# Optimization experiments

Measured on AMD Instinct MI355X. Metric: run time of the kernel, lower is better.

Reference implementation:

```python
import jax, jax.numpy as jnp
import numpy as np

EPS = 1e-5  # BatchNorm1d default eps


def _proj_bn(x, W, gamma, beta, mean, var):
    # Conv1d(kernel=1, bias=False) == channel matmul, then inference BatchNorm1d.
    y = jnp.einsum('oc,bcn->bon', W, x)  # (B, C_out, N)
    scale = gamma / jnp.sqrt(var + EPS)  # (C_out,)
    shift = beta - mean * scale
    return y * scale[:, None] + shift[:, None]


def setup_inputs() -> dict:
    key = jax.random.key(0)
    ks = jax.random.split(key, 8)
    B, C, N = 8, 512, 2048
    inp = {
        'input': jax.random.normal(ks[0], (B, C, N), dtype=jnp.float32),
        'Wq': jax.random.normal(ks[1], (C, C), dtype=jnp.float32) * (1.0 / np.sqrt(C)),
        'gq': jnp.ones((C,), jnp.float32),
        'bq': jnp.zeros((C,), jnp.float32),
        'mq': jax.random.normal(ks[2], (C,), dtype=jnp.float32) * 0.1,
        'vq': jax.random.uniform(ks[3], (C,), dtype=jnp.float32) + 0.5,
        'Wk': jax.random.normal(ks[4], (C, C), dtype=jnp.float32) * (1.0 / np.sqrt(C)),
        'gk': jnp.ones((C,), jnp.float32),
        'bk': jnp.zeros((C,), jnp.float32),
        'mk': jax.random.normal(ks[5], (C,), dtype=jnp.float32) * 0.1,
        'vk': jax.random.uniform(ks[6], (C,), dtype=jnp.float32) + 0.5,
        'Wv': jax.random.normal(ks[7], (C, C), dtype=jnp.float32) * (1.0 / np.sqrt(C)),
        'gv': jnp.ones((C,), jnp.float32),
        'bv': jnp.zeros((C,), jnp.float32),
        'mv': jax.random.normal(jax.random.fold_in(key, 100), (C,), dtype=jnp.float32) * 0.1,
        'vv': jax.random.uniform(jax.random.fold_in(key, 101), (C,), dtype=jnp.float32) + 0.5,
    }
    return inp


def reference(input, Wq, gq, bq, mq, vq, Wk, gk, bk, mk, vk, Wv, gv, bv, mv, vv):
    q = _proj_bn(input, Wq, gq, bq, mq, vq)  # (B, C, N)
    k = _proj_bn(input, Wk, gk, bk, mk, vk)
    v = _proj_bn(input, Wv, gv, bv, mv, vv)
    # w[b, i, j] = sum_c q[b, c, i] * k[b, c, j]
    w = jnp.einsum('bci,bcj->bij', q, k)
    a = jax.nn.softmax(w, axis=-1)  # softmax over key axis j (dim 3 in torch)
    # c[b, c, i] = sum_j a[b, i, j] * v[b, c, j]  (== (v * w.softmax(3)).sum(3))
    return jnp.einsum('bij,bcj->bci', a, v)
```

## Files before the change

kernel.cpp:

```cpp
#include <hip/hip_runtime.h>
#include <cstdint>
#include <cstddef>

#define EPSV 1e-5f
constexpr int B_ = 8;
constexpr int C_ = 512;
constexpr int N_ = 2048;

typedef _Float16 f16x8 __attribute__((ext_vector_type(8)));
typedef float    f32x4 __attribute__((ext_vector_type(4)));

__device__ __forceinline__ unsigned short f16b(float f) {
    _Float16 h = (_Float16)f;
    return __builtin_bit_cast(unsigned short, h);
}

__device__ __forceinline__ void gload_lds16(const void* g, void* l) {
    __builtin_amdgcn_global_load_lds(
        (const __attribute__((address_space(1))) void*)g,
        (__attribute__((address_space(3))) void*)l, 16, 0, 0);
}

__global__ __launch_bounds__(256) void split_x_kernel(
    const float* __restrict__ x, unsigned short* __restrict__ xh)
{
    __shared__ float T[64][65];
    const int b = blockIdx.z, c0 = blockIdx.y * 64, n0 = blockIdx.x * 64;
    const float* xb = x + ((size_t)b * C_ + c0) * N_ + n0;
    const int tid = threadIdx.x;
    const int lr = tid >> 4;
    const int lcn = (tid & 15) * 4;
#pragma unroll
    for (int it = 0; it < 4; ++it) {
        float4 v = *(const float4*)&xb[(size_t)(lr + 16 * it) * N_ + lcn];
        T[lr + 16 * it][lcn + 0] = v.x;
        T[lr + 16 * it][lcn + 1] = v.y;
        T[lr + 16 * it][lcn + 2] = v.z;
        T[lr + 16 * it][lcn + 3] = v.w;
    }
    __syncthreads();
    const int n = tid >> 2, cb = (tid & 3) * 16;
    alignas(16) unsigned short h[16];
#pragma unroll
    for (int i = 0; i < 16; ++i)
        h[i] = f16b(T[cb + i][n]);
    const size_t o = ((size_t)b * N_ + n0 + n) * C_ + c0 + cb;
    *(uint4*)&xh[o]     = *(uint4*)&h[0];
    *(uint4*)&xh[o + 8] = *(uint4*)&h[8];
}

__global__ __launch_bounds__(256) void split_w_kernel(
    const float* __restrict__ W, unsigned short* __restrict__ wh)
{
    const int i = (blockIdx.x * 256 + threadIdx.x) * 4;
    float4 v = *(const float4*)&W[i];
    alignas(8) unsigned short h[4];
    h[0] = f16b(v.x); h[1] = f16b(v.y); h[2] = f16b(v.z); h[3] = f16b(v.w);
    *(ushort4*)&wh[i] = *(ushort4*)&h[0];
}

__global__ __launch_bounds__(512) void param_concat_kernel(
    const float* gq, const float* bq, const float* mq, const float* vq,
    const float* gk, const float* bk, const float* mk, const float* vk,
    float* sg, float* sb, float* sm, float* sv)
{
    const int i = threadIdx.x;
    sg[i] = gq[i];       sg[512 + i] = gk[i];
    sb[i] = bq[i];       sb[512 + i] = bk[i];
    sm[i] = mq[i];       sm[512 + i] = mk[i];
    sv[i] = vq[i];       sv[512 + i] = vk[i];
}

__global__ __launch_bounds__(256) void projv_mfma(
    const unsigned short* __restrict__ Ah, const unsigned short* __restrict__ Bh,
    int M, int N, int K, int lda, int ldb,
    long strideA, long strideB, long strideC,
    void* __restrict__ C0,
    const float* __restrict__ g, const float* __restrict__ bt,
    const float* __restrict__ mu, const float* __restrict__ var)
{
    __shared__ char smem[16384];

    const int id = blockIdx.x;
    const int bz = id & 7;
    const int s  = id >> 3;
    const int bx = s & 3, by = s >> 2;
    const int n0 = bx * 128;
    const int m0 = by * 128;

    const unsigned short* Ahb = Ah + (size_t)bz * strideA;
    const unsigned short* Bhb = Bh + (size_t)bz * strideB;

    const int tid = threadIdx.x;
    const int lane = tid & 63;
    const int wv = tid >> 6;
    const int wr = wv >> 1, wc = wv & 1;
    const int l4 = lane >> 4, l15 = lane & 15;
    const int srow = lane >> 2, scol8 = (lane & 3) * 8;

    f32x4 acc[4][4] = {};

    for (int k0 = 0; k0 < K; k0 += 32) {
#pragma unroll
        for (int cc = 0; cc < 2; ++cc) {
            const int c = wv * 2 + cc;
            const size_t aoff = (size_t)(m0 + c * 16 + srow) * lda + k0 + scol8;
            const size_t boff = (size_t)(n0 + c * 16 + srow) * ldb + k0 + scol8;
            gload_lds16(Ahb + aoff, smem + c * 1024);
            gload_lds16(Bhb + boff, smem + 8192 + c * 1024);
        }
        __syncthreads();

        f16x8 ah[4], bh[4];
#pragma unroll
        for (int f = 0; f < 4; ++f) {
            const int arow = wr * 64 + f * 16 + l15;
            const int brow = wc * 64 + f * 16 + l15;
            ah[f] = *(const f16x8*)(smem + arow * 64 + l4 * 16);
            bh[f] = *(const f16x8*)(smem + 8192 + brow * 64 + l4 * 16);
        }
#pragma unroll
        for (int fm = 0; fm < 4; ++fm)
#pragma unroll
            for (int fn = 0; fn < 4; ++fn)
                acc[fm][fn] = __builtin_amdgcn_mfma_f32_16x16x32_f16(
                    ah[fm], bh[fn], acc[fm][fn], 0, 0, 0);
        __syncthreads();
    }

#pragma unroll
    for (int fm = 0; fm < 4; ++fm) {
#pragma unroll
        for (int fn = 0; fn < 4; ++fn) {
            const int m = m0 + wr * 64 + fm * 16 + l4 * 4;
            const int n = n0 + wc * 64 + fn * 16 + l15;
            unsigned short* H = (unsigned short*)C0 + (size_t)bz * strideC;
            const float sc = g[n] * rsqrtf(var[n] + EPSV);
            const float sh = bt[n] - mu[n] * sc;
            alignas(8) unsigned short h4[4];
#pragma unroll
            for (int r = 0; r < 4; ++r)
                h4[r] = f16b(acc[fm][fn][r] * sc + sh);
            *(ushort4*)&H[(size_t)n * M + m] = *(ushort4*)&h4[0];
        }
    }
}

constexpr int EPI_QK = 0, EPI_PROJT = 2;

template <int EPI>
__global__ __launch_bounds__(512, 2) void qk256(
    const unsigned short* __restrict__ Ah, const unsigned short* __restrict__ Bh,
    int M, int N, int K, int lda, int ldb,
    long strideA, long strideB, long strideC,
    void* __restrict__ C0, float* __restrict__ ML,
    const float* __restrict__ g, const float* __restrict__ bt,
    const float* __restrict__ mu, const float* __restrict__ var)
{
    __shared__ char smem[131072];

    const int id = blockIdx.x;
    const int bz = id & 7;
    const int s  = id >> 3;
    const int bx = s & 7, by = s >> 3;
    const int n0 = bx * 256;
    const int m0 = by * 256;

    const unsigned short* Ahb = Ah + (size_t)bz * strideA;
    const unsigned short* Bhb = Bh + (size_t)bz * strideB;

    const int tid  = threadIdx.x;
    const int lane = tid & 63;
    const int wv   = tid >> 6;
    const int wr   = wv >> 2, wc = wv & 3;
    const int WRB  = wr * 128, WCB = wc * 64;
    const int l4 = lane >> 4, l15 = lane & 15;

    const int srow  = tid >> 3;
    const int sslot = ((tid & 7) ^ (srow & 7)) * 8;

#define STAGE(t)                                                              \
    {                                                                         \
        char* dst = smem + ((t) & 1) * 65536;                                 \
        const unsigned short* asrc =                                          \
            Ahb + (size_t)(m0 + srow) * lda + (t) * 64 + sslot;               \
        _Pragma("unroll")                                                     \
        for (int u = 0; u < 4; ++u)                                           \
            gload_lds16(asrc + (size_t)(u * 64) * lda,                        \
                        dst + u * 8192 + tid * 16);                           \
        const unsigned short* bsrc =                                          \
            Bhb + (size_t)(n0 + srow) * ldb + (t) * 64 + sslot;               \
        _Pragma("unroll")                                                     \
        for (int u = 0; u < 4; ++u)                                           \
            gload_lds16(bsrc + (size_t)(u * 64) * ldb,                        \
                        dst + 32768 + u * 8192 + tid * 16);                   \
    }

    f32x4 acc[8][4] = {};
    const int NT = K / 64;

    STAGE(0);

    for (int t = 0; t < NT; ++t) {
        char* cur = smem + (t & 1) * 65536;
        __builtin_amdgcn_s_barrier();
        if (t + 1 < NT) {
            STAGE(t + 1);
            asm volatile("s_waitcnt vmcnt(8)" ::: "memory");
        } else {
            asm volatile("s_waitcnt vmcnt(0)" ::: "memory");
        }
        __builtin_amdgcn_s_barrier();

        f16x8 ah[8][2], bh[4][2];
#pragma unroll
        for (int m = 0; m < 8; ++m) {
            const int row = WRB + m * 16 + l15;
#pragma unroll
            for (int kk = 0; kk < 2; ++kk)
                ah[m][kk] = *(const f16x8*)(cur + row * 128 +
                                            (((kk << 2) | l4) ^ (row & 7)) * 16);
        }
#pragma unroll
        for (int n = 0; n < 4; ++n) {
            const int row = WCB + n * 16 + l15;
#pragma unroll
            for (int kk = 0; kk < 2; ++kk)
                bh[n][kk] = *(const f16x8*)(cur + 32768 + row * 128 +
                                            (((kk << 2) | l4) ^ (row & 7)) * 16);
        }
        __builtin_amdgcn_s_setprio(1);
#pragma unroll
        for (int kk = 0; kk < 2; ++kk)
#pragma unroll
            for (int m = 0; m < 8; ++m)
#pragma unroll
                for (int n = 0; n < 4; ++n)
                    acc[m][n] = __builtin_amdgcn_mfma_f32_16x16x32_f16(
                        ah[m][kk], bh[n][kk], acc[m][n], 0, 0, 0);
        __builtin_amdgcn_s_setprio(0);
    }
#undef STAGE

    if constexpr (EPI == EPI_QK) {
        unsigned short* H = (unsigned short*)C0 + (size_t)bz * strideC;
        const int tcol = bx * 4 + wc;
        const size_t mbase = (((size_t)bz * 32 + tcol) * 2) * 2048;
#pragma unroll
        for (int m = 0; m < 8; ++m) {
#pragma unroll
            for (int r = 0; r < 4; ++r) {
                float mx = fmaxf(fmaxf(acc[m][0][r], acc[m][1][r]),
                                 fmaxf(acc[m][2][r], acc[m][3][r]));
#pragma unroll
                for (int off = 1; off < 16; off <<= 1)
                    mx = fmaxf(mx, __shfl_xor(mx, off));
                float pe[4];
                float s2 = 0.f;
#pragma unroll
                for (int n = 0; n < 4; ++n) {
                    pe[n] = __expf(acc[m][n][r] - mx);
                    s2 += pe[n];
                }
#pragma unroll
                for (int off = 1; off < 16; off <<= 1)
                    s2 += __shfl_xor(s2, off);
                const int rloc = WRB + m * 16 + l4 * 4 + r;
                if (l15 == 0) {
                    ML[mbase + m0 + rloc] = mx;
                    ML[mbase + 2048 + m0 + rloc] = s2;
                }
#pragma unroll
                for (int n = 0; n < 4; ++n)
                    H[(size_t)(m0 + rloc) * 2048 + n0 + WCB + n * 16 + l15] =
                        f16b(pe[n]);
            }
        }
    } else {
        unsigned short* H = (unsigned short*)C0 + (size_t)bz * strideC;
#pragma unroll
        for (int m = 0; m < 8; ++m) {
            const int mg = m0 + WRB + m * 16 + l4 * 4;
            float sc[4], sh[4];
#pragma unroll
            for (int r = 0; r < 4; ++r) {
                const int o = mg + r;
                sc[r] = g[o] * rsqrtf(var[o] + EPSV);
                sh[r] = bt[o] - mu[o] * sc[r];
            }
#pragma unroll
            for (int n = 0; n < 4; ++n) {
                const int ng = n0 + WCB + n * 16 + l15;
                alignas(8) unsigned short h4[4];
#pragma unroll
                for (int r = 0; r < 4; ++r)
                    h4[r] = f16b(acc[m][n][r] * sc[r] + sh[r]);
                *(ushort4*)&H[(size_t)ng * M + mg] = *(ushort4*)&h4[0];
            }
        }
    }
}

__global__ __launch_bounds__(512, 2) void pv256(
    const unsigned short* __restrict__ Ah, const unsigned short* __restrict__ Bh,
    int K, int lda, int ldb, long strideA, long strideB, long strideC,
    void* __restrict__ C0,
    const float* __restrict__ corr, const float* __restrict__ linv)
{
    constexpr int BUFSZ = 49152;
    __shared__ char smem[163840];

    const int id = blockIdx.x;
    const int bz = id & 7;
    const int s  = id >> 3;
    const int bx = s & 3, by = s >> 2;
    const int n0 = bx * 128;
    const int m0 = by * 256;

    const unsigned short* Ahb = Ah + (size_t)bz * strideA;
    const unsigned short* Bhb = Bh + (size_t)bz * strideB;

    const int tid  = threadIdx.x;
    const int lane = tid & 63;
    const int wv   = tid >> 6;
    const int wr   = wv >> 2, wc = wv & 3;
    const int WRB  = wr * 128, WCB = wc * 32;
    const int l4 = lane >> 4, l15 = lane & 15;

    const int srow = tid >> 3;
    const int sslot = ((tid & 7) ^ (srow & 7)) * 8;

    unsigned short* corrLds = (unsigned short*)(smem + 147456);
    for (int idx = tid; idx < 2048; idx += 512) {
        const int t = idx >> 6, i4 = (idx & 63) * 4;
        float4 c4 = *(const float4*)&corr[((size_t)bz * 32 + t) * 2048 + m0 + i4];
        alignas(8) unsigned short h4[4] =
            {f16b(c4.x), f16b(c4.y), f16b(c4.z), f16b(c4.w)};
        *(ushort4*)&corrLds[(size_t)t * 256 + i4] = *(ushort4*)&h4[0];
    }
    __syncthreads();

#define STAGE(t)                                                              \
    {                                                                         \
        char* dst = smem + ((t) % 3) * BUFSZ;                                 \
        const unsigned short* asrc =                                          \
            Ahb + (size_t)(m0 + srow) * lda + (t) * 64 + sslot;               \
        _Pragma("unroll")                                                     \
        for (int u = 0; u < 4; ++u)                                           \
            gload_lds16(asrc + (size_t)(u * 64) * lda,                        \
                        dst + u * 8192 + tid * 16);                           \
        const unsigned short* bsrc =                                          \
            Bhb + (size_t)(n0 + srow) * ldb + (t) * 64 + sslot;               \
        _Pragma("unroll")                                                     \
        for (int u = 0; u < 2; ++u)                                           \
            gload_lds16(bsrc + (size_t)(u * 64) * ldb,                        \
                        dst + 32768 + u * 8192 + tid * 16);                   \
    }

    f32x4 acc[8][2] = {};
    const int NT = K / 64;

    STAGE(0);
    STAGE(1);

    for (int t = 0; t < NT; ++t) {
        char* cur = smem + (t % 3) * BUFSZ;
        if (t + 2 < NT) {
            asm volatile("s_waitcnt vmcnt(6)" ::: "memory");
        } else {
            asm volatile("s_waitcnt vmcnt(0)" ::: "memory");
        }
        __builtin_amdgcn_s_barrier();
        asm volatile("" ::: "memory");
        if (t + 2 < NT) STAGE(t + 2);

        f16x8 ah[8][2], bh[2][2];
#pragma unroll
        for (int m = 0; m < 8; ++m) {
            const int row = WRB + m * 16 + l15;
#pragma unroll
            for (int kk = 0; kk < 2; ++kk)
                ah[m][kk] = *(const f16x8*)(cur + row * 128 +
                                            (((kk << 2) | l4) ^ (row & 7)) * 16);
        }
#pragma unroll
        for (int n = 0; n < 2; ++n) {
            const int row = WCB + n * 16 + l15;
#pragma unroll
            for (int kk = 0; kk < 2; ++kk)
                bh[n][kk] = *(const f16x8*)(cur + 32768 + row * 128 +
                                            (((kk << 2) | l4) ^ (row & 7)) * 16);
        }
#pragma unroll
        for (int m = 0; m < 8; ++m) {
            const _Float16 cf = ((const _Float16*)corrLds)
                [(size_t)t * 256 + WRB + m * 16 + l15];
            ah[m][0] = ah[m][0] * cf;
            ah[m][1] = ah[m][1] * cf;
        }
        __builtin_amdgcn_s_setprio(1);
#pragma unroll
        for (int kk = 0; kk < 2; ++kk)
#pragma unroll
            for (int m = 0; m < 8; ++m)
#pragma unroll
                for (int n = 0; n < 2; ++n)
                    acc[m][n] = __builtin_amdgcn_mfma_f32_16x16x32_f16(
                        ah[m][kk], bh[n][kk], acc[m][n], 0, 0, 0);
        __builtin_amdgcn_s_setprio(0);
    }
#undef STAGE

    float* Cb = (float*)C0 + (size_t)bz * strideC;
    const float* lb = linv + (size_t)bz * 2048;
#pragma unroll
    for (int m = 0; m < 8; ++m) {
        const int mrow = m0 + WRB + m * 16 + l4 * 4;
        float lv[4];
#pragma unroll
        for (int r = 0; r < 4; ++r)
            lv[r] = lb[mrow + r];
#pragma unroll
        for (int n = 0; n < 2; ++n) {
            const int col = n0 + WCB + n * 16 + l15;
            float4 o4 = make_float4(acc[m][n][0] * lv[0],
                                    acc[m][n][1] * lv[1],
                                    acc[m][n][2] * lv[2],
                                    acc[m][n][3] * lv[3]);
            *(float4*)&Cb[(size_t)col * 2048 + mrow] = o4;
        }
    }
}

__global__ __launch_bounds__(256) void ml_combine_kernel(
    const float* __restrict__ ml, float* __restrict__ corr,
    float* __restrict__ linv)
{
    const int idx = blockIdx.x * 256 + threadIdx.x;
    const int b = idx >> 11, i = idx & 2047;
    const float* base = ml + ((size_t)b * 32) * 2 * 2048 + i;
    float M = -3.0e38f;
#pragma unroll 8
    for (int t = 0; t < 32; ++t)
        M = fmaxf(M, base[(size_t)t * 4096]);
    float L = 0.f;
    float* cb = corr + (size_t)b * 32 * 2048 + i;
#pragma unroll 8
    for (int t = 0; t < 32; ++t) {
        const float c = __expf(base[(size_t)t * 4096] - M);
        L += c * base[(size_t)t * 4096 + 2048];
        cb[(size_t)t * 2048] = c;
    }
    linv[idx] = 1.0f / L;
}

extern "C" void kernel_launch(void* const* d_in, const int* in_sizes, int n_in,
                              void* d_out, int out_size, void* d_ws, size_t ws_size,
                              hipStream_t stream)
{
    (void)in_sizes; (void)n_in; (void)out_size; (void)ws_size;
    const float* x  = (const float*)d_in[0];
    const float* Wq = (const float*)d_in[1];
    const float* gq = (const float*)d_in[2];
    const float* bq = (const float*)d_in[3];
    const float* mq = (const float*)d_in[4];
    const float* vq = (const float*)d_in[5];
    const float* Wk = (const float*)d_in[6];
    const float* gk = (const float*)d_in[7];
    const float* bk = (const float*)d_in[8];
    const float* mk = (const float*)d_in[9];
    const float* vk = (const float*)d_in[10];
    const float* Wv = (const float*)d_in[11];
    const float* gv = (const float*)d_in[12];
    const float* bv = (const float*)d_in[13];
    const float* mv = (const float*)d_in[14];
    const float* vv = (const float*)d_in[15];
    float* out = (float*)d_out;

    const size_t MiB = 1048576;
    char* ws = (char*)d_ws;
    unsigned short* Wqh = (unsigned short*)(ws + 0 * 524288);
    unsigned short* Wkh = (unsigned short*)(ws + 1 * 524288);
    unsigned short* Wvh = (unsigned short*)(ws + 2 * 524288);
    unsigned short* vbf  = (unsigned short*)(ws + 2 * MiB);
    unsigned short* qkTh = (unsigned short*)(ws + 18 * MiB);
    unsigned short* xTh  = (unsigned short*)(ws + 50 * MiB);
    unsigned short* pbuf = (unsigned short*)(ws + 66 * MiB);
    float* mlbuf = (float*)(ws + 130 * MiB);
    float* corr  = (float*)(ws + 134 * MiB);
    float* linv  = (float*)(ws + 136 * MiB);
    float* sg = (float*)(ws + 136 * MiB + 65536);
    float* sb = sg + 1024;
    float* sm = sb + 1024;
    float* sv = sm + 1024;

    const long BS = (long)N_ * C_;
    const long QKS = (long)N_ * 1024;

    split_x_kernel<<<dim3(N_ / 64, C_ / 64, B_), 256, 0, stream>>>(x, xTh);
    split_w_kernel<<<dim3(256), 256, 0, stream>>>(Wq, Wqh);
    split_w_kernel<<<dim3(256), 256, 0, stream>>>(Wk, Wkh);
    split_w_kernel<<<dim3(256), 256, 0, stream>>>(Wv, Wvh);
    param_concat_kernel<<<dim3(1), 512, 0, stream>>>(
        gq, bq, mq, vq, gk, bk, mk, vk, sg, sb, sm, sv);

    qk256<EPI_PROJT><<<dim3(256), 512, 0, stream>>>(
        Wqh, xTh, 1024, 2048, 512, 512, 512, 0, BS, QKS, qkTh,
        nullptr, sg, sb, sm, sv);

    projv_mfma<<<dim3(512), 256, 0, stream>>>(
        xTh, Wvh, 2048, 512, 512, 512, 512, BS, 0, BS, vbf,
        gv, bv, mv, vv);

    qk256<EPI_QK><<<dim3(512), 512, 0, stream>>>(
        qkTh, qkTh + 512, 2048, 2048, 512, 1024, 1024, QKS, QKS,
        (long)N_ * N_, pbuf, mlbuf, nullptr, nullptr, nullptr, nullptr);

    ml_combine_kernel<<<dim3(B_ * N_ / 256), 256, 0, stream>>>(
        mlbuf, corr, linv);

    pv256<<<dim3(256), 512, 0, stream>>>(
        pbuf, vbf, 2048, 2048, 2048, (long)N_ * N_, BS, BS, out, corr, linv);
}
```

Measured before the change: 179.7 us.

## Split GEMM main loops into finer-grained quarter-tile stages with interleaved barriers

Restructures the qk256 and pv256 main loops so each K-tile is split into half-K sub-buffers with a 32-column swizzled LDS layout. Global-to-LDS loads are issued in quarter (qk) or half (pv) chunks between MFMA clusters, and each cluster is fenced by barriers with priority raising. This is a ping-pong style schedule that overlaps LDS reads, async global loads and MFMA more finely. pv256 moves from a triple to a double buffer, which lowers its LDS footprint. The intricate vmcnt accounting risks races or stalls if any count is wrong.

```diff
diff --git a/kernel.cpp b/kernel.cpp
--- a/kernel.cpp
+++ b/kernel.cpp
@@ -146,6 +146,15 @@
     }
 }
 
+#define BAR_PRE()                                                             \
+    __builtin_amdgcn_s_barrier();                                             \
+    asm volatile("s_waitcnt lgkmcnt(0)" ::: "memory");                        \
+    __builtin_amdgcn_sched_barrier(0);                                        \
+    __builtin_amdgcn_s_setprio(1)
+#define BAR_POST()                                                            \
+    __builtin_amdgcn_s_setprio(0);                                            \
+    __builtin_amdgcn_s_barrier()
+
 constexpr int EPI_QK = 0, EPI_PROJT = 2;
 
 template <int EPI>
@@ -176,71 +185,79 @@
     const int WRB  = wr * 128, WCB = wc * 64;
     const int l4 = lane >> 4, l15 = lane & 15;
 
-    const int srow  = tid >> 3;
-    const int sslot = ((tid & 7) ^ (srow & 7)) * 8;
-
-#define STAGE(t)                                                              \
-    {                                                                         \
-        char* dst = smem + ((t) & 1) * 65536;                                 \
-        const unsigned short* asrc =                                          \
-            Ahb + (size_t)(m0 + srow) * lda + (t) * 64 + sslot;               \
+    const int NT = K / 64;
+
+#define ISSUE_Q(sv_)                                                          \
+    if ((sv_) < 4 * NT) {                                                     \
+        const int T__ = (sv_) >> 2, j__ = (sv_) & 3;                          \
+        char* rb = smem + (T__ & 1) * 65536 + ((j__ & 1) ? 32768 : 0) +       \
+                   ((j__ >> 1) * 16384);                                      \
+        const unsigned short* src = (j__ & 1) ? Bhb : Ahb;                    \
+        const int base0 = (j__ & 1) ? n0 : m0;                                \
+        const int ld = (j__ & 1) ? ldb : lda;                                 \
+        const int colb = T__ * 64 + (j__ >> 1) * 32;                          \
         _Pragma("unroll")                                                     \
-        for (int u = 0; u < 4; ++u)                                           \
-            gload_lds16(asrc + (size_t)(u * 64) * lda,                        \
-                        dst + u * 8192 + tid * 16);                           \
-        const unsigned short* bsrc =                                          \
-            Bhb + (size_t)(n0 + srow) * ldb + (t) * 64 + sslot;               \
+        for (int u = 0; u < 2; ++u) {                                         \
+            const int L = u * 512 + tid;                                      \
+            const int row = L >> 2;                                           \
+            gload_lds16(src + (size_t)(base0 + row) * ld + colb +             \
+                            (((tid & 3) ^ (row & 3)) * 8),                    \
+                        rb + L * 16);                                         \
+        }                                                                     \
+    }
+
+#define RDA(kk, dst)                                                          \
+    _Pragma("unroll")                                                         \
+    for (int m_ = 0; m_ < 8; ++m_) {                                          \
+        const int r_ = WRB + m_ * 16 + l15;                                   \
+        dst[m_] = *(const f16x8*)(cur + (kk) * 16384 + r_ * 64 +              \
+                                  ((l4 ^ (r_ & 3)) * 16));                    \
+    }
+#define RDB(kk, nlo, dst)                                                     \
+    _Pragma("unroll")                                                         \
+    for (int n_ = 0; n_ < 2; ++n_) {                                          \
+        const int r_ = WCB + ((nlo) + n_) * 16 + l15;                         \
+        dst[n_] = *(const f16x8*)(cur + 32768 + (kk) * 16384 + r_ * 64 +      \
+                                  ((l4 ^ (r_ & 3)) * 16));                    \
+    }
+#define MFM(nlo)                                                              \
+    _Pragma("unroll")                                                         \
+    for (int m_ = 0; m_ < 8; ++m_)                                            \
         _Pragma("unroll")                                                     \
-        for (int u = 0; u < 4; ++u)                                           \
-            gload_lds16(bsrc + (size_t)(u * 64) * ldb,                        \
-                        dst + 32768 + u * 8192 + tid * 16);                   \
-    }
+        for (int n_ = 0; n_ < 2; ++n_)                                        \
+            acc[m_][(nlo) + n_] = __builtin_amdgcn_mfma_f32_16x16x32_f16(     \
+                ah[m_], bq[n_], acc[m_][(nlo) + n_], 0, 0, 0);
 
     f32x4 acc[8][4] = {};
-    const int NT = K / 64;
-
-    STAGE(0);
+    f16x8 ah[8], bq[2];
+
+    ISSUE_Q(0); ISSUE_Q(1); ISSUE_Q(2); ISSUE_Q(3); ISSUE_Q(4);
+    asm volatile("s_waitcnt vmcnt(6)" ::: "memory");
+    __builtin_amdgcn_s_barrier();
 
     for (int t = 0; t < NT; ++t) {
         char* cur = smem + (t & 1) * 65536;
-        __builtin_amdgcn_s_barrier();
-        if (t + 1 < NT) {
-            STAGE(t + 1);
-            asm volatile("s_waitcnt vmcnt(8)" ::: "memory");
-        } else {
-            asm volatile("s_waitcnt vmcnt(0)" ::: "memory");
-        }
-        __builtin_amdgcn_s_barrier();
-
-        f16x8 ah[8][2], bh[4][2];
-#pragma unroll
-        for (int m = 0; m < 8; ++m) {
-            const int row = WRB + m * 16 + l15;
-#pragma unroll
-            for (int kk = 0; kk < 2; ++kk)
-                ah[m][kk] = *(const f16x8*)(cur + row * 128 +
-                                            (((kk << 2) | l4) ^ (row & 7)) * 16);
-        }
-#pragma unroll
-        for (int n = 0; n < 4; ++n) {
-            const int row = WCB + n * 16 + l15;
-#pragma unroll
-            for (int kk = 0; kk < 2; ++kk)
-                bh[n][kk] = *(const f16x8*)(cur + 32768 + row * 128 +
-                                            (((kk << 2) | l4) ^ (row & 7)) * 16);
-        }
-        __builtin_amdgcn_s_setprio(1);
-#pragma unroll
-        for (int kk = 0; kk < 2; ++kk)
-#pragma unroll
-            for (int m = 0; m < 8; ++m)
-#pragma unroll
-                for (int n = 0; n < 4; ++n)
-                    acc[m][n] = __builtin_amdgcn_mfma_f32_16x16x32_f16(
-                        ah[m][kk], bh[n][kk], acc[m][n], 0, 0, 0);
-        __builtin_amdgcn_s_setprio(0);
-    }
-#undef STAGE
+        RDA(0, ah); RDB(0, 0, bq);
+        ISSUE_Q(4 * t + 5);
+        BAR_PRE(); MFM(0); BAR_POST();
+        RDB(0, 2, bq);
+        ISSUE_Q(4 * t + 6);
+        if (t + 1 < NT) { asm volatile("s_waitcnt vmcnt(6)" ::: "memory"); }
+        else            { asm volatile("s_waitcnt vmcnt(0)" ::: "memory"); }
+        BAR_PRE(); MFM(2); BAR_POST();
+        RDA(1, ah); RDB(1, 0, bq);
+        ISSUE_Q(4 * t + 7);
+        BAR_PRE(); MFM(0); BAR_POST();
+        RDB(1, 2, bq);
+        ISSUE_Q(4 * t + 8);
+        if (t + 2 < NT)       { asm volatile("s_waitcnt vmcnt(6)" ::: "memory"); }
+        else if (t + 2 == NT) { asm volatile("s_waitcnt vmcnt(4)" ::: "memory"); }
+        BAR_PRE(); MFM(2); BAR_POST();
+    }
+#undef ISSUE_Q
+#undef RDA
+#undef RDB
+#undef MFM
 
     if constexpr (EPI == EPI_QK) {
         unsigned short* H = (unsigned short*)C0 + (size_t)bz * strideC;
@@ -307,8 +324,7 @@
     void* __restrict__ C0,
     const float* __restrict__ corr, const float* __restrict__ linv)
 {
-    constexpr int BUFSZ = 49152;
-    __shared__ char smem[163840];
+    __shared__ char smem[114688];
 
     const int id = blockIdx.x;
     const int bz = id & 7;
@@ -327,10 +343,9 @@
     const int WRB  = wr * 128, WCB = wc * 32;
     const int l4 = lane >> 4, l15 = lane & 15;
 
-    const int srow = tid >> 3;
-    const int sslot = ((tid & 7) ^ (srow & 7)) * 8;
-
-    unsigned short* corrLds = (unsigned short*)(smem + 147456);
+    const int NT = K / 64;
+
+    unsigned short* corrLds = (unsigned short*)(smem + 98304);
     for (int idx = tid; idx < 2048; idx += 512) {
         const int t = idx >> 6, i4 = (idx & 63) * 4;
         float4 c4 = *(const float4*)&corr[((size_t)bz * 32 + t) * 2048 + m0 + i4];
@@ -340,76 +355,81 @@
     }
     __syncthreads();
 
-#define STAGE(t)                                                              \
-    {                                                                         \
-        char* dst = smem + ((t) % 3) * BUFSZ;                                 \
-        const unsigned short* asrc =                                          \
-            Ahb + (size_t)(m0 + srow) * lda + (t) * 64 + sslot;               \
+#define ISSUE_P(sv_)                                                          \
+    if ((sv_) < 2 * NT) {                                                     \
+        const int T__ = (sv_) >> 1, h__ = (sv_) & 1;                          \
+        char* rb = smem + (T__ & 1) * 49152;                                  \
+        const int colb = T__ * 64 + h__ * 32;                                 \
         _Pragma("unroll")                                                     \
-        for (int u = 0; u < 4; ++u)                                           \
-            gload_lds16(asrc + (size_t)(u * 64) * lda,                        \
-                        dst + u * 8192 + tid * 16);                           \
-        const unsigned short* bsrc =                                          \
-            Bhb + (size_t)(n0 + srow) * ldb + (t) * 64 + sslot;               \
+        for (int u = 0; u < 2; ++u) {                                         \
+            const int L = u * 512 + tid;                                      \
+            const int row = L >> 2;                                           \
+            gload_lds16(Ahb + (size_t)(m0 + row) * lda + colb +               \
+                            (((tid & 3) ^ (row & 3)) * 8),                    \
+                        rb + h__ * 16384 + L * 16);                           \
+        }                                                                     \
+        {                                                                     \
+            const int row = tid >> 2;                                         \
+            gload_lds16(Bhb + (size_t)(n0 + row) * ldb + colb +               \
+                            (((tid & 3) ^ (row & 3)) * 8),                    \
+                        rb + 32768 + h__ * 8192 + tid * 16);                  \
+        }                                                                     \
+    }
+
+#define RDAP(kk)                                                              \
+    _Pragma("unroll")                                                         \
+    for (int m_ = 0; m_ < 8; ++m_) {                                          \
+        const int r_ = WRB + m_ * 16 + l15;                                   \
+        ah[m_] = *(const f16x8*)(cur + (kk) * 16384 + r_ * 64 +               \
+                                 ((l4 ^ (r_ & 3)) * 16));                     \
+    }
+#define RDBP(kk)                                                              \
+    _Pragma("unroll")                                                         \
+    for (int n_ = 0; n_ < 2; ++n_) {                                          \
+        const int r_ = WCB + n_ * 16 + l15;                                   \
+        bq[n_] = *(const f16x8*)(cur + 32768 + (kk) * 8192 + r_ * 64 +        \
+                                 ((l4 ^ (r_ & 3)) * 16));                     \
+    }
+#define CORRM(t)                                                              \
+    _Pragma("unroll")                                                         \
+    for (int m_ = 0; m_ < 8; ++m_) {                                          \
+        const _Float16 cf = ((const _Float16*)corrLds)                        \
+            [(size_t)(t) * 256 + WRB + m_ * 16 + l15];                        \
+        ah[m_] = ah[m_] * cf;                                                 \
+    }
+#define MFMP()                                                                \
+    _Pragma("unroll")                                                         \
+    for (int m_ = 0; m_ < 8; ++m_)                                            \
         _Pragma("unroll")                                                     \
-        for (int u = 0; u < 2; ++u)                                           \
-            gload_lds16(bsrc + (size_t)(u * 64) * ldb,                        \
-                        dst + 32768 + u * 8192 + tid * 16);                   \
-    }
+        for (int n_ = 0; n_ < 2; ++n_)                                        \
+            acc[m_][n_] = __builtin_amdgcn_mfma_f32_16x16x32_f16(             \
+                ah[m_], bq[n_], acc[m_][n_], 0, 0, 0);
 
     f32x4 acc[8][2] = {};
-    const int NT = K / 64;
-
-    STAGE(0);
-    STAGE(1);
+    f16x8 ah[8], bq[2];
+
+    ISSUE_P(0); ISSUE_P(1); ISSUE_P(2);
+    asm volatile("s_waitcnt vmcnt(6)" ::: "memory");
+    __builtin_amdgcn_s_barrier();
 
     for (int t = 0; t < NT; ++t) {
-        char* cur = smem + (t % 3) * BUFSZ;
-        if (t + 2 < NT) {
-            asm volatile("s_waitcnt vmcnt(6)" ::: "memory");
-        } else {
-            asm volatile("s_waitcnt vmcnt(0)" ::: "memory");
-        }
-        __builtin_amdgcn_s_barrier();
-        asm volatile("" ::: "memory");
-        if (t + 2 < NT) STAGE(t + 2);
-
-        f16x8 ah[8][2], bh[2][2];
-#pragma unroll
-        for (int m = 0; m < 8; ++m) {
-            const int row = WRB + m * 16 + l15;
-#pragma unroll
-            for (int kk = 0; kk < 2; ++kk)
-                ah[m][kk] = *(const f16x8*)(cur + row * 128 +
-                                            (((kk << 2) | l4) ^ (row & 7)) * 16);
-        }
-#pragma unroll
-        for (int n = 0; n < 2; ++n) {
-            const int row = WCB + n * 16 + l15;
-#pragma unroll
-            for (int kk = 0; kk < 2; ++kk)
-                bh[n][kk] = *(const f16x8*)(cur + 32768 + row * 128 +
-                                            (((kk << 2) | l4) ^ (row & 7)) * 16);
-        }
-#pragma unroll
-        for (int m = 0; m < 8; ++m) {
-            const _Float16 cf = ((const _Float16*)corrLds)
-                [(size_t)t * 256 + WRB + m * 16 + l15];
-            ah[m][0] = ah[m][0] * cf;
-            ah[m][1] = ah[m][1] * cf;
-        }
-        __builtin_amdgcn_s_setprio(1);
-#pragma unroll
-        for (int kk = 0; kk < 2; ++kk)
-#pragma unroll
-            for (int m = 0; m < 8; ++m)
-#pragma unroll
-                for (int n = 0; n < 2; ++n)
-                    acc[m][n] = __builtin_amdgcn_mfma_f32_16x16x32_f16(
-                        ah[m][kk], bh[n][kk], acc[m][n], 0, 0, 0);
-        __builtin_amdgcn_s_setprio(0);
-    }
-#undef STAGE
+        char* cur = smem + (t & 1) * 49152;
+        RDAP(0); RDBP(0); CORRM(t);
+        ISSUE_P(2 * t + 3);
+        if (t + 1 < NT) { asm volatile("s_waitcnt vmcnt(6)" ::: "memory"); }
+        else            { asm volatile("s_waitcnt vmcnt(0)" ::: "memory"); }
+        BAR_PRE(); MFMP(); BAR_POST();
+        RDAP(1); RDBP(1); CORRM(t);
+        ISSUE_P(2 * t + 4);
+        if (t + 2 < NT)       { asm volatile("s_waitcnt vmcnt(6)" ::: "memory"); }
+        else if (t + 2 == NT) { asm volatile("s_waitcnt vmcnt(3)" ::: "memory"); }
+        BAR_PRE(); MFMP(); BAR_POST();
+    }
+#undef ISSUE_P
+#undef RDAP
+#undef RDBP
+#undef CORRM
+#undef MFMP
 
     float* Cb = (float*)C0 + (size_t)bz * strideC;
     const float* lb = linv + (size_t)bz * 2048;
```

New measurement: 201.3 us. 1.12x slower.

## Fuse V projection into the stacked Q/K projection GEMM launch

Applied to the files above, without the earlier changes.

Removes the separate small-tile projv_mfma kernel and stacks Wq, Wk and Wv into one contiguous weight matrix. The existing 256x256 qk256 projection kernel now runs over 1536 output rows (384 blocks), with a branch in the epilogue that writes V rows to the vbf buffer. This removes one launch and reuses the larger, more efficient tile for V. In exchange, the V epilogue stores each f16 element as a scalar, with lanes of a row writing consecutive addresses, where the Q/K path uses ushort4 vector stores, so V output writes may be less efficient.

```diff
diff --git a/kernel.cpp b/kernel.cpp
--- a/kernel.cpp
+++ b/kernel.cpp
@@ -62,88 +62,14 @@
 __global__ __launch_bounds__(512) void param_concat_kernel(
     const float* gq, const float* bq, const float* mq, const float* vq,
     const float* gk, const float* bk, const float* mk, const float* vk,
+    const float* gv, const float* bv, const float* mv, const float* vv,
     float* sg, float* sb, float* sm, float* sv)
 {
     const int i = threadIdx.x;
-    sg[i] = gq[i];       sg[512 + i] = gk[i];
-    sb[i] = bq[i];       sb[512 + i] = bk[i];
-    sm[i] = mq[i];       sm[512 + i] = mk[i];
-    sv[i] = vq[i];       sv[512 + i] = vk[i];
-}
-
-__global__ __launch_bounds__(256) void projv_mfma(
-    const unsigned short* __restrict__ Ah, const unsigned short* __restrict__ Bh,
-    int M, int N, int K, int lda, int ldb,
-    long strideA, long strideB, long strideC,
-    void* __restrict__ C0,
-    const float* __restrict__ g, const float* __restrict__ bt,
-    const float* __restrict__ mu, const float* __restrict__ var)
-{
-    __shared__ char smem[16384];
-
-    const int id = blockIdx.x;
-    const int bz = id & 7;
-    const int s  = id >> 3;
-    const int bx = s & 3, by = s >> 2;
-    const int n0 = bx * 128;
-    const int m0 = by * 128;
-
-    const unsigned short* Ahb = Ah + (size_t)bz * strideA;
-    const unsigned short* Bhb = Bh + (size_t)bz * strideB;
-
-    const int tid = threadIdx.x;
-    const int lane = tid & 63;
-    const int wv = tid >> 6;
-    const int wr = wv >> 1, wc = wv & 1;
-    const int l4 = lane >> 4, l15 = lane & 15;
-    const int srow = lane >> 2, scol8 = (lane & 3) * 8;
-
-    f32x4 acc[4][4] = {};
-
-    for (int k0 = 0; k0 < K; k0 += 32) {
-#pragma unroll
-        for (int cc = 0; cc < 2; ++cc) {
-            const int c = wv * 2 + cc;
-            const size_t aoff = (size_t)(m0 + c * 16 + srow) * lda + k0 + scol8;
-            const size_t boff = (size_t)(n0 + c * 16 + srow) * ldb + k0 + scol8;
-            gload_lds16(Ahb + aoff, smem + c * 1024);
-            gload_lds16(Bhb + boff, smem + 8192 + c * 1024);
-        }
-        __syncthreads();
-
-        f16x8 ah[4], bh[4];
-#pragma unroll
-        for (int f = 0; f < 4; ++f) {
-            const int arow = wr * 64 + f * 16 + l15;
-            const int brow = wc * 64 + f * 16 + l15;
-            ah[f] = *(const f16x8*)(smem + arow * 64 + l4 * 16);
-            bh[f] = *(const f16x8*)(smem + 8192 + brow * 64 + l4 * 16);
-        }
-#pragma unroll
-        for (int fm = 0; fm < 4; ++fm)
-#pragma unroll
-            for (int fn = 0; fn < 4; ++fn)
-                acc[fm][fn] = __builtin_amdgcn_mfma_f32_16x16x32_f16(
-                    ah[fm], bh[fn], acc[fm][fn], 0, 0, 0);
-        __syncthreads();
-    }
-
-#pragma unroll
-    for (int fm = 0; fm < 4; ++fm) {
-#pragma unroll
-        for (int fn = 0; fn < 4; ++fn) {
-            const int m = m0 + wr * 64 + fm * 16 + l4 * 4;
-            const int n = n0 + wc * 64 + fn * 16 + l15;
-            unsigned short* H = (unsigned short*)C0 + (size_t)bz * strideC;
-            const float sc = g[n] * rsqrtf(var[n] + EPSV);
-            const float sh = bt[n] - mu[n] * sc;
-            alignas(8) unsigned short h4[4];
-#pragma unroll
-            for (int r = 0; r < 4; ++r)
-                h4[r] = f16b(acc[fm][fn][r] * sc + sh);
-            *(ushort4*)&H[(size_t)n * M + m] = *(ushort4*)&h4[0];
-        }
-    }
+    sg[i] = gq[i];  sg[512 + i] = gk[i];  sg[1024 + i] = gv[i];
+    sb[i] = bq[i];  sb[512 + i] = bk[i];  sb[1024 + i] = bv[i];
+    sm[i] = mq[i];  sm[512 + i] = mk[i];  sm[1024 + i] = mv[i];
+    sv[i] = vq[i];  sv[512 + i] = vk[i];  sv[1024 + i] = vv[i];
 }
 
 constexpr int EPI_QK = 0, EPI_PROJT = 2;
@@ -151,9 +77,9 @@
 template <int EPI>
 __global__ __launch_bounds__(512, 2) void qk256(
     const unsigned short* __restrict__ Ah, const unsigned short* __restrict__ Bh,
-    int M, int N, int K, int lda, int ldb,
-    long strideA, long strideB, long strideC,
-    void* __restrict__ C0, float* __restrict__ ML,
+    int K, int lda, int ldb,
+    long strideA, long strideB, long strideC, long strideC2,
+    void* __restrict__ C0, void* __restrict__ C1, float* __restrict__ ML,
     const float* __restrict__ g, const float* __restrict__ bt,
     const float* __restrict__ mu, const float* __restrict__ var)
 {
@@ -277,25 +203,49 @@
             }
         }
     } else {
-        unsigned short* H = (unsigned short*)C0 + (size_t)bz * strideC;
-#pragma unroll
-        for (int m = 0; m < 8; ++m) {
-            const int mg = m0 + WRB + m * 16 + l4 * 4;
-            float sc[4], sh[4];
-#pragma unroll
-            for (int r = 0; r < 4; ++r) {
-                const int o = mg + r;
-                sc[r] = g[o] * rsqrtf(var[o] + EPSV);
-                sh[r] = bt[o] - mu[o] * sc[r];
+        if (m0 < 1024) {
+            unsigned short* H = (unsigned short*)C0 + (size_t)bz * strideC;
+#pragma unroll
+            for (int m = 0; m < 8; ++m) {
+                const int mg = m0 + WRB + m * 16 + l4 * 4;
+                float sc[4], sh[4];
+#pragma unroll
+                for (int r = 0; r < 4; ++r) {
+                    const int o = mg + r;
+                    sc[r] = g[o] * rsqrtf(var[o] + EPSV);
+                    sh[r] = bt[o] - mu[o] * sc[r];
+                }
+#pragma unroll
+                for (int n = 0; n < 4; ++n) {
+                    const int ng = n0 + WCB + n * 16 + l15;
+                    alignas(8) unsigned short h4[4];
+#pragma unroll
+                    for (int r = 0; r < 4; ++r)
+                        h4[r] = f16b(acc[m][n][r] * sc[r] + sh[r]);
+                    *(ushort4*)&H[(size_t)ng * 1024 + mg] = *(ushort4*)&h4[0];
+                }
             }
-#pragma unroll
-            for (int n = 0; n < 4; ++n) {
-                const int ng = n0 + WCB + n * 16 + l15;
-                alignas(8) unsigned short h4[4];
-#pragma unroll
-                for (int r = 0; r < 4; ++r)
-                    h4[r] = f16b(acc[m][n][r] * sc[r] + sh[r]);
-                *(ushort4*)&H[(size_t)ng * M + mg] = *(ushort4*)&h4[0];
+        } else {
+            unsigned short* V = (unsigned short*)C1 + (size_t)bz * strideC2;
+#pragma unroll
+            for (int m = 0; m < 8; ++m) {
+                const int mg = m0 + WRB + m * 16 + l4 * 4;
+                float sc[4], sh[4];
+#pragma unroll
+                for (int r = 0; r < 4; ++r) {
+                    const int o = mg + r;
+                    sc[r] = g[o] * rsqrtf(var[o] + EPSV);
+                    sh[r] = bt[o] - mu[o] * sc[r];
+                }
+                const int d0 = mg - 1024;
+#pragma unroll
+                for (int n = 0; n < 4; ++n) {
+                    const int ng = n0 + WCB + n * 16 + l15;
+#pragma unroll
+                    for (int r = 0; r < 4; ++r)
+                        V[(size_t)(d0 + r) * 2048 + ng] =
+                            f16b(acc[m][n][r] * sc[r] + sh[r]);
+                }
             }
         }
     }
@@ -479,9 +429,10 @@
 
     const size_t MiB = 1048576;
     char* ws = (char*)d_ws;
-    unsigned short* Wqh = (unsigned short*)(ws + 0 * 524288);
-    unsigned short* Wkh = (unsigned short*)(ws + 1 * 524288);
-    unsigned short* Wvh = (unsigned short*)(ws + 2 * 524288);
+    unsigned short* Wst = (unsigned short*)(ws);
+    unsigned short* Wqh = Wst;
+    unsigned short* Wkh = Wst + 512 * 512;
+    unsigned short* Wvh = Wst + 1024 * 512;
     unsigned short* vbf  = (unsigned short*)(ws + 2 * MiB);
     unsigned short* qkTh = (unsigned short*)(ws + 18 * MiB);
     unsigned short* xTh  = (unsigned short*)(ws + 50 * MiB);
@@ -490,9 +441,9 @@
     float* corr  = (float*)(ws + 134 * MiB);
     float* linv  = (float*)(ws + 136 * MiB);
     float* sg = (float*)(ws + 136 * MiB + 65536);
-    float* sb = sg + 1024;
-    float* sm = sb + 1024;
-    float* sv = sm + 1024;
+    float* sb = sg + 1536;
+    float* sm = sb + 1536;
+    float* sv = sm + 1536;
 
     const long BS = (long)N_ * C_;
     const long QKS = (long)N_ * 1024;
@@ -502,19 +453,15 @@
     split_w_kernel<<<dim3(256), 256, 0, stream>>>(Wk, Wkh);
     split_w_kernel<<<dim3(256), 256, 0, stream>>>(Wv, Wvh);
     param_concat_kernel<<<dim3(1), 512, 0, stream>>>(
-        gq, bq, mq, vq, gk, bk, mk, vk, sg, sb, sm, sv);
-
-    qk256<EPI_PROJT><<<dim3(256), 512, 0, stream>>>(
-        Wqh, xTh, 1024, 2048, 512, 512, 512, 0, BS, QKS, qkTh,
+        gq, bq, mq, vq, gk, bk, mk, vk, gv, bv, mv, vv, sg, sb, sm, sv);
+
+    qk256<EPI_PROJT><<<dim3(384), 512, 0, stream>>>(
+        Wst, xTh, 512, 512, 512, 0, BS, QKS, BS, qkTh, vbf,
         nullptr, sg, sb, sm, sv);
 
-    projv_mfma<<<dim3(512), 256, 0, stream>>>(
-        xTh, Wvh, 2048, 512, 512, 512, 512, BS, 0, BS, vbf,
-        gv, bv, mv, vv);
-
     qk256<EPI_QK><<<dim3(512), 512, 0, stream>>>(
-        qkTh, qkTh + 512, 2048, 2048, 512, 1024, 1024, QKS, QKS,
-        (long)N_ * N_, pbuf, mlbuf, nullptr, nullptr, nullptr, nullptr);
+        qkTh, qkTh + 512, 512, 1024, 1024, QKS, QKS, (long)N_ * N_, 0,
+        pbuf, nullptr, mlbuf, nullptr, nullptr, nullptr, nullptr);
 
     ml_combine_kernel<<<dim3(B_ * N_ / 256), 256, 0, stream>>>(
         mlbuf, corr, linv);
```

New measurement: 176.9 us. Within noise of the previous version (-1.6%).
